# Optimization experiments

Hardware: AMD Instinct MI355X
Metric: run time of the kernel (lower is better)

The kernel has to match this reference:

```python
import jax, jax.numpy as jnp
import numpy as np

LOG2PI = float(np.log(2.0 * np.pi))


def setup_inputs() -> dict:
    key = jax.random.key(0)
    k1, k2, k3 = jax.random.split(key, 3)
    N, D = 2048, 64
    z = jax.random.normal(k1, (N, D), dtype=jnp.float32)
    z_mean = jax.random.normal(k2, (N, D), dtype=jnp.float32)
    z_log_squared_scale = jax.random.normal(k3, (N, D), dtype=jnp.float32)
    return {"z": z, "z_mean": z_mean, "z_log_squared_scale": z_log_squared_scale}


def gaussian_log_density(samples, mean, log_var):
    # log N(samples; mean, exp(log_var)), elementwise per dim
    inv_var = jnp.exp(-log_var)
    diff = samples - mean
    return -0.5 * (diff * diff * inv_var + log_var + LOG2PI)


def reference(z, z_mean, z_log_squared_scale):
    # Pairwise log q(z_i | x_j) per latent dim: [N, N, D]
    log_qz_prob = gaussian_log_density(
        z[:, None, :], z_mean[None, :, :], z_log_squared_scale[None, :, :]
    )
    # sum_d logsumexp_j  -> log prod_d q(z_d)
    log_qz_product = jnp.sum(jax.scipy.special.logsumexp(log_qz_prob, axis=1), axis=1)
    # logsumexp_j sum_d  -> log q(z)
    log_qz = jax.scipy.special.logsumexp(jnp.sum(log_qz_prob, axis=2), axis=1)
    return jnp.mean(log_qz_product - log_qz)
```

## Files before the change

kernel.cpp:

```cpp
#include <hip/hip_runtime.h>
#include <hip/hip_fp16.h>
#include <math.h>
#include <stdint.h>

#define LOG2E  1.44269504088896340736f
#define LN2    0.69314718055994530942f
#define LOG2PI 1.8378770664093453f

#define NN 2048
#define DD 64

#define BIAS_F   16252928.0f
#define KBIT     2205910303u
#define CLAMP_LO 8388608.0f
#define CLAMP_HI 16777215.0f

#define C1250H 0x64E264E2u
#define KK16   0x63DC63DCu
#define SHL5   0x00050005u
#define SELA   0x01000100u
#define SELB   0x03020302u

typedef short          bf16x8 __attribute__((ext_vector_type(8)));
typedef float          f32x16 __attribute__((ext_vector_type(16)));

union PkU { uint32_t u; __half h[2]; };

__device__ __forceinline__ float fexp2(float x) { return __builtin_amdgcn_exp2f(x); }
__device__ __forceinline__ float flog2(float x) { return __builtin_amdgcn_logf(x); }
__device__ __forceinline__ unsigned short f2bf(float f) {
    uint32_t u = __float_as_uint(f);
    u += 0x7FFFu + ((u >> 16) & 1u);
    return (unsigned short)(u >> 16);
}
__device__ __forceinline__ float ubf(unsigned short s) {
    return __uint_as_float((uint32_t)s << 16);
}
__device__ __forceinline__ uint32_t bfpack(float a, float b) {
    return (uint32_t)f2bf(a) | ((uint32_t)f2bf(b) << 16);
}
__device__ __forceinline__ uint32_t h1(float x) {
    return (uint32_t)__half_as_ushort(__float2half_rn(x));
}
__device__ __forceinline__ uint32_t hdup(float x) { uint32_t t = h1(x); return t | (t << 16); }
__device__ __forceinline__ uint32_t hpack(float a, float b) { return h1(a) | (h1(b) << 16); }

__device__ __forceinline__ uint32_t pk_fma(uint32_t a, uint32_t b, uint32_t c) {
    uint32_t d;
    asm("v_pk_fma_f16 %0, %1, %2, %3" : "=v"(d) : "v"(a), "v"(b), "v"(c));
    return d;
}
__device__ __forceinline__ uint32_t pk_nfma(uint32_t a, uint32_t b, uint32_t c) {
    uint32_t d;
    asm("v_pk_fma_f16 %0, %1, %2, %3 neg_lo:[1,0,0] neg_hi:[1,0,0]"
        : "=v"(d) : "v"(a), "v"(b), "v"(c));
    return d;
}
__device__ __forceinline__ uint32_t pk_max(uint32_t a, uint32_t b) {
    uint32_t d;
    asm("v_pk_max_f16 %0, %1, %2" : "=v"(d) : "v"(a), "v"(b));
    return d;
}
__device__ __forceinline__ uint32_t pk_addf(uint32_t a, uint32_t b) {
    uint32_t d;
    asm("v_pk_add_f16 %0, %1, %2" : "=v"(d) : "v"(a), "v"(b));
    return d;
}
__device__ __forceinline__ uint32_t pk_shl(uint32_t a, uint32_t sh) {
    uint32_t d;
    asm("v_pk_lshlrev_b16 %0, %1, %2" : "=v"(d) : "v"(sh), "v"(a));
    return d;
}
__device__ __forceinline__ uint32_t pk_addu(uint32_t a, uint32_t b) {
    uint32_t d;
    asm("v_pk_add_u16 %0, %1, %2" : "=v"(d) : "v"(a), "v"(b));
    return d;
}
__device__ __forceinline__ uint32_t perm(uint32_t src, uint32_t sel) {
    uint32_t d;
    asm("v_perm_b32 %0, %1, %2, %3" : "=v"(d) : "v"(src), "v"(src), "v"(sel));
    return d;
}

__global__ __launch_bounds__(256) void k1(
    const float* __restrict__ z, const float* __restrict__ zm,
    const float* __restrict__ zlv,
    uint2* __restrict__ smC2,
    uint32_t* __restrict__ pqfH, uint32_t* __restrict__ pqfL,
    uint32_t* __restrict__ zfH, uint32_t* __restrict__ zfL,
    float* __restrict__ CjS, uint32_t* __restrict__ zpkT)
{
    __shared__ float L[32][65];
    int tid = threadIdx.x, lane = tid & 63, row = tid >> 6;

    if (blockIdx.x < 128) {
        int jb = blockIdx.x * 16;
        #pragma unroll
        for (int c = 0; c < 4; ++c) {
            int j   = jb + c * 4 + row;
            int idx = j * DD + lane;
            float mean = zm[idx], lv = zlv[idx];
            float p   = -0.72134752f * fexp2(-lv * LOG2E);
            float q   = -2.0f * mean * p;
            float c22 = -0.72134752f * (lv + LOG2PI);
            float sp  = 5.65685424f * __builtin_sqrtf(-p);
            float msp = -mean * sp;
            float Cp  = fmaf(32.0f, c22, 1952.0f);
            smC2[idx] = make_uint2(hpack(sp, msp), hdup(Cp));
            unsigned short hp = f2bf(p), hq = f2bf(q);
            pqfH[idx] = (uint32_t)hp | ((uint32_t)hq << 16);
            pqfL[idx] = bfpack(p - ubf(hp), q - ubf(hq));
            float t = fmaf(mean * mean, p, c22);
            #pragma unroll
            for (int off = 32; off; off >>= 1) t += __shfl_xor(t, off, 64);
            if (lane == 0) CjS[j] = fmaf(t + 64.0f, 65536.0f, BIAS_F);
        }
    } else {
        int ib = (blockIdx.x - 128) * 32;
        #pragma unroll
        for (int c = 0; c < 8; ++c) {
            int il  = c * 4 + row;
            int idx = (ib + il) * DD + lane;
            float zv = z[idx];
            L[il][lane] = zv;
            float z2 = zv * zv;
            unsigned short hz2 = f2bf(z2), hz = f2bf(zv);
            zfH[idx] = (uint32_t)hz2 | ((uint32_t)hz << 16);
            zfL[idx] = bfpack(z2 - ubf(hz2), zv - ubf(hz));
        }
        __syncthreads();
        #pragma unroll
        for (int k = 0; k < 4; ++k) {
            int e = k * 256 + tid;
            int u = e & 7, d = (e >> 3) & 63, itl = e >> 9;
            float za = L[itl * 16 + 2 * u][d];
            float zb = L[itl * 16 + 2 * u + 1][d];
            zpkT[((ib >> 4) + itl) * 512 + d * 8 + u] = hpack(za, zb);
        }
    }
}

__global__ __launch_bounds__(512) void kw(
    const uint2* __restrict__ smC2, const uint32_t* __restrict__ zpkT,
    const uint32_t* __restrict__ zfH, const uint32_t* __restrict__ zfL,
    const uint32_t* __restrict__ pqfH, const uint32_t* __restrict__ pqfL,
    const float* __restrict__ CjS,
    uint32_t* __restrict__ sums, float* __restrict__ k2part)
{
    __shared__ float shbuf[2048];
    int tid = threadIdx.x, lane = tid & 63, w = tid >> 6;

    if (blockIdx.x < 512) {
        int it = blockIdx.x >> 2, jsl = blockIdx.x & 3;
        int j0 = jsl * 512 + (w & 3) * 64 + (w >> 2) * 256;

        uint32_t zpk[8], acc[8];
        #pragma unroll
        for (int u = 0; u < 8; ++u) {
            zpk[u] = zpkT[it * 512 + lane * 8 + u];
            acc[u] = 0u;
        }
        uint32_t kk = KK16, sh5 = SHL5, clf = C1250H, sA = SELA, sB = SELB;
        asm volatile("" : "+v"(kk), "+v"(sh5), "+v"(clf), "+v"(sA), "+v"(sB));

        const uint2* sp2 = smC2 + (size_t)j0 * DD + lane;
        #pragma unroll 4
        for (int jj = 0; jj < 64; ++jj) {
            uint2 v = sp2[(size_t)jj * DD];
            uint32_t sd = perm(v.x, sA);
            uint32_t md = perm(v.x, sB);
            #pragma unroll
            for (int u = 0; u < 8; ++u) {
                uint32_t wp = pk_fma(zpk[u], sd, md);
                uint32_t y  = pk_nfma(wp, wp, v.y);
                y = pk_max(y, clf);
                uint32_t e = pk_addu(pk_shl(y, sh5), kk);
                acc[u] = pk_addf(acc[u], e);
            }
        }

        uint32_t* sl = (uint32_t*)shbuf;
        if (w < 4) {
            #pragma unroll
            for (int u = 0; u < 8; ++u) sl[(w * 8 + u) * 64 + lane] = acc[u];
        }
        __syncthreads();
        if (w >= 4) {
            int slice = jsl * 4 + (w - 4);
            #pragma unroll
            for (int u = 0; u < 8; ++u) {
                PkU a, b;
                a.u = acc[u];
                b.u = sl[((w - 4) * 8 + u) * 64 + lane];
                float lo = __half2float(a.h[0]) + __half2float(b.h[0]);
                float hi = __half2float(a.h[1]) + __half2float(b.h[1]);
                sums[((size_t)slice * 1024 + it * 8 + u) * 64 + lane] =
                    hpack(lo * 0.0625f, hi * 0.0625f);
            }
        }
    } else {
        float* cjsL = shbuf;
        for (int t = tid; t < NN; t += 512) cjsL[t] = CjS[t];
        __syncthreads();

        int gid = (blockIdx.x - 512) * 8 + w;
        int it = gid >> 5, jg = gid & 31;
        int l31 = lane & 31, h = lane >> 5;

        const char* zbH = (const char*)zfH + (size_t)(it * 32 + l31) * 256 + h * 16;
        const char* zbL = (const char*)zfL + (size_t)(it * 32 + l31) * 256 + h * 16;
        bf16x8 BH[8], BL[8];
        #pragma unroll
        for (int kc = 0; kc < 8; ++kc) {
            BH[kc] = *(const bf16x8*)(zbH + kc * 32);
            BL[kc] = *(const bf16x8*)(zbL + kc * 32);
        }

        float isum = 0.0f;
        #pragma unroll
        for (int t4 = 0; t4 < 2; ++t4) {
            int jt = jg * 2 + t4;
            const char* abH = (const char*)pqfH + (size_t)(jt * 32 + l31) * 256 + h * 16;
            const char* abL = (const char*)pqfL + (size_t)(jt * 32 + l31) * 256 + h * 16;
            f32x16 acc;
            #pragma unroll
            for (int r = 0; r < 16; ++r) acc[r] = 0.0f;
            #pragma unroll
            for (int kc = 0; kc < 8; ++kc) {
                bf16x8 AH = *(const bf16x8*)(abH + kc * 32);
                bf16x8 AL = *(const bf16x8*)(abL + kc * 32);
                acc = __builtin_amdgcn_mfma_f32_32x32x16_bf16(AH, BH[kc], acc, 0, 0, 0);
                acc = __builtin_amdgcn_mfma_f32_32x32x16_bf16(AH, BL[kc], acc, 0, 0, 0);
                acc = __builtin_amdgcn_mfma_f32_32x32x16_bf16(AL, BH[kc], acc, 0, 0, 0);
            }
            #pragma unroll
            for (int r = 0; r < 16; ++r) {
                int R = (r & 3) + 8 * (r >> 2) + 4 * h;
                float y = fmaf(acc[r], 65536.0f, cjsL[jt * 32 + R]);
                y = fminf(fmaxf(y, CLAMP_LO), CLAMP_HI);
                isum += __uint_as_float((__float_as_uint(y) << 7) + KBIT);
            }
        }
        isum += __shfl_xor(isum, 32, 64);
        if (lane < 32) k2part[(size_t)jg * NN + it * 32 + l31] = isum;
    }
}

__global__ __launch_bounds__(256) void k5(
    const __half* __restrict__ sums, const float* __restrict__ k2part,
    float* __restrict__ diff)
{
    int lane = threadIdx.x & 63, w = threadIdx.x >> 6;
    int i = blockIdx.x * 4 + w;
    int ip = i >> 1, hsel = i & 1;

    float tot = 0.0f;
    #pragma unroll
    for (int q = 0; q < 16; ++q)
        tot += __half2float(sums[(((size_t)q * 1024 + ip) * 64 + lane) * 2 + hsel]);
    float t = flog2(tot);
    #pragma unroll
    for (int off = 32; off; off >>= 1) t += __shfl_xor(t, off, 64);

    float s2 = (lane < 32) ? k2part[(size_t)lane * NN + i] : 0.0f;
    #pragma unroll
    for (int off = 32; off; off >>= 1) s2 += __shfl_xor(s2, off, 64);

    if (lane == 0) diff[i] = LN2 * (t - flog2(s2) - 128.0f);
}

__global__ __launch_bounds__(256) void k6(
    const float* __restrict__ diff, float* __restrict__ out)
{
    __shared__ float red[256];
    int tid = threadIdx.x;
    float t = 0.0f;
    for (int k = tid; k < NN; k += 256) t += diff[k];
    red[tid] = t;
    __syncthreads();
    #pragma unroll
    for (int off = 128; off; off >>= 1) {
        if (tid < off) red[tid] += red[tid + off];
        __syncthreads();
    }
    if (tid == 0) out[0] = red[0] * (1.0f / (float)NN);
}

extern "C" void kernel_launch(void* const* d_in, const int* in_sizes, int n_in,
                              void* d_out, int out_size, void* d_ws, size_t ws_size,
                              hipStream_t stream)
{
    const float* z   = (const float*)d_in[0];
    const float* zm  = (const float*)d_in[1];
    const float* zlv = (const float*)d_in[2];
    float* out = (float*)d_out;

    char* b = (char*)d_ws;
    uint2*    smC2 = (uint2*)(b);
    uint32_t* pqfH = (uint32_t*)(b + (1 << 20));
    uint32_t* pqfL = (uint32_t*)(b + (1 << 20) + (512 << 10));
    uint32_t* zfH  = (uint32_t*)(b + (2 << 20));
    uint32_t* zfL  = (uint32_t*)(b + (2 << 20) + (512 << 10));
    uint32_t* zpkT = (uint32_t*)(b + (3 << 20));
    float*    CjS  = (float*)(b + (3 << 20) + (256 << 10));
    uint32_t* sums = (uint32_t*)(b + (3 << 20) + (512 << 10));
    float*    k2p  = (float*)(b + (7 << 20) + (512 << 10));
    float*    diff = (float*)(b + (7 << 20) + (768 << 10));

    k1<<<192, 256, 0, stream>>>(z, zm, zlv, smC2, pqfH, pqfL, zfH, zfL, CjS, zpkT);
    kw<<<768, 512, 0, stream>>>(smC2, zpkT, zfH, zfL, pqfH, pqfL, CjS, sums, k2p);
    k5<<<512, 256, 0, stream>>>((const __half*)sums, k2p, diff);
    k6<<<1,   256, 0, stream>>>(diff, out);
}
```

Before: 51.71 us.

## Register-tile 16 rows per wave in pairwise kernel with LDS four-wave reduction

Each wave of the packed-half pairwise pass now keeps 16 z rows in registers and sweeps 32 j values, instead of 8 rows over 64 j. Each smC2 load is therefore reused across twice as many packed FMA chains. Blocks shrink to 256 threads, and all four waves' partial sums are reduced through shared memory before the 1/16-scaled results are written to the same sums layout. The grid and wave indexing of the second (matrix) branch are adjusted to keep the same work mapping. The cost is doubled accumulator and z registers, which may lower occupancy, plus a wider LDS reduction.

```diff
diff --git a/kernel.cpp b/kernel.cpp
--- a/kernel.cpp
+++ b/kernel.cpp
@@ -140,37 +140,37 @@
     }
 }
 
-__global__ __launch_bounds__(512) void kw(
+__global__ __launch_bounds__(256) void kw(
     const uint2* __restrict__ smC2, const uint32_t* __restrict__ zpkT,
     const uint32_t* __restrict__ zfH, const uint32_t* __restrict__ zfL,
     const uint32_t* __restrict__ pqfH, const uint32_t* __restrict__ pqfL,
     const float* __restrict__ CjS,
     uint32_t* __restrict__ sums, float* __restrict__ k2part)
 {
-    __shared__ float shbuf[2048];
+    __shared__ uint32_t shbuf[4096];
     int tid = threadIdx.x, lane = tid & 63, w = tid >> 6;
 
-    if (blockIdx.x < 512) {
-        int it = blockIdx.x >> 2, jsl = blockIdx.x & 3;
-        int j0 = jsl * 512 + (w & 3) * 64 + (w >> 2) * 256;
-
-        uint32_t zpk[8], acc[8];
-        #pragma unroll
-        for (int u = 0; u < 8; ++u) {
-            zpk[u] = zpkT[it * 512 + lane * 8 + u];
+    if (blockIdx.x < 1024) {
+        int it = blockIdx.x >> 4, jb = blockIdx.x & 15;
+        int j0 = jb * 128 + w * 32;
+
+        uint32_t zpk[16], acc[16];
+        #pragma unroll
+        for (int u = 0; u < 16; ++u) {
+            zpk[u] = zpkT[(2 * it + (u >> 3)) * 512 + lane * 8 + (u & 7)];
             acc[u] = 0u;
         }
         uint32_t kk = KK16, sh5 = SHL5, clf = C1250H, sA = SELA, sB = SELB;
         asm volatile("" : "+v"(kk), "+v"(sh5), "+v"(clf), "+v"(sA), "+v"(sB));
 
         const uint2* sp2 = smC2 + (size_t)j0 * DD + lane;
-        #pragma unroll 4
-        for (int jj = 0; jj < 64; ++jj) {
+        #pragma unroll 2
+        for (int jj = 0; jj < 32; ++jj) {
             uint2 v = sp2[(size_t)jj * DD];
             uint32_t sd = perm(v.x, sA);
             uint32_t md = perm(v.x, sB);
             #pragma unroll
-            for (int u = 0; u < 8; ++u) {
+            for (int u = 0; u < 16; ++u) {
                 uint32_t wp = pk_fma(zpk[u], sd, md);
                 uint32_t y  = pk_nfma(wp, wp, v.y);
                 y = pk_max(y, clf);
@@ -179,31 +179,29 @@
             }
         }
 
-        uint32_t* sl = (uint32_t*)shbuf;
-        if (w < 4) {
-            #pragma unroll
-            for (int u = 0; u < 8; ++u) sl[(w * 8 + u) * 64 + lane] = acc[u];
-        }
+        #pragma unroll
+        for (int u = 0; u < 16; ++u) shbuf[(w * 16 + u) * 64 + lane] = acc[u];
         __syncthreads();
-        if (w >= 4) {
-            int slice = jsl * 4 + (w - 4);
-            #pragma unroll
-            for (int u = 0; u < 8; ++u) {
-                PkU a, b;
-                a.u = acc[u];
-                b.u = sl[((w - 4) * 8 + u) * 64 + lane];
-                float lo = __half2float(a.h[0]) + __half2float(b.h[0]);
-                float hi = __half2float(a.h[1]) + __half2float(b.h[1]);
-                sums[((size_t)slice * 1024 + it * 8 + u) * 64 + lane] =
-                    hpack(lo * 0.0625f, hi * 0.0625f);
+        #pragma unroll
+        for (int k = 0; k < 4; ++k) {
+            int e = k * 256 + tid;
+            int u = e >> 6, d = e & 63;
+            float lo = 0.0f, hi = 0.0f;
+            #pragma unroll
+            for (int w2 = 0; w2 < 4; ++w2) {
+                PkU a; a.u = shbuf[(w2 * 16 + u) * 64 + d];
+                lo += __half2float(a.h[0]);
+                hi += __half2float(a.h[1]);
             }
+            sums[((size_t)jb * 1024 + it * 16 + u) * 64 + d] =
+                hpack(lo * 0.0625f, hi * 0.0625f);
         }
     } else {
-        float* cjsL = shbuf;
-        for (int t = tid; t < NN; t += 512) cjsL[t] = CjS[t];
+        float* cjsL = (float*)shbuf;
+        for (int t = tid; t < NN; t += 256) cjsL[t] = CjS[t];
         __syncthreads();
 
-        int gid = (blockIdx.x - 512) * 8 + w;
+        int gid = (blockIdx.x - 1024) * 4 + w;
         int it = gid >> 5, jg = gid & 31;
         int l31 = lane & 31, h = lane >> 5;
 
@@ -307,8 +305,8 @@
     float*    k2p  = (float*)(b + (7 << 20) + (512 << 10));
     float*    diff = (float*)(b + (7 << 20) + (768 << 10));
 
-    k1<<<192, 256, 0, stream>>>(z, zm, zlv, smC2, pqfH, pqfL, zfH, zfL, CjS, zpkT);
-    kw<<<768, 512, 0, stream>>>(smC2, zpkT, zfH, zfL, pqfH, pqfL, CjS, sums, k2p);
-    k5<<<512, 256, 0, stream>>>((const __half*)sums, k2p, diff);
-    k6<<<1,   256, 0, stream>>>(diff, out);
-}
+    k1<<<192,  256, 0, stream>>>(z, zm, zlv, smC2, pqfH, pqfL, zfH, zfL, CjS, zpkT);
+    kw<<<1536, 256, 0, stream>>>(smC2, zpkT, zfH, zfL, pqfH, pqfL, CjS, sums, k2p);
+    k5<<<512,  256, 0, stream>>>((const __half*)sums, k2p, diff);
+    k6<<<1,    256, 0, stream>>>(diff, out);
+}
```

Measured after the change: 49.03 us. -5.2%, faster.
